# Kernel tuning notes

Measured on AMD Instinct MI355X. Metric: run time of the kernel, lower is better.

Reference implementation:

```python
import jax, jax.numpy as jnp
import numpy as np

RHO = 1e-8
EPS = 1e-8
THRESH = 0.9
MARK = -2


def maxi(x):
    # keep only the max entry along last dim, zero elsewhere
    idx = jnp.argmax(x, axis=-1, keepdims=True)
    return jnp.where(jnp.arange(x.shape[-1]) == idx, x, 0.0)


def argmaxi(x, eps=EPS):
    mx = jnp.abs(maxi(x))
    factors = jnp.max(mx, axis=-1, keepdims=True) - eps
    return mx / factors


def outer_forward(mm0, xs, rho=RHO):
    # mm0: (fields, mems, dim), xs: (batch, fields, dim)
    m = mm0 - 0.5
    x = xs - 0.5
    num = jnp.einsum('fmd,bfd->bfm', m, x) * 0.5
    m_norm = jnp.sqrt(jnp.sum(m * m, axis=-1))            # (f, m)
    x_norm = jnp.sqrt(jnp.sum(x * x, axis=-1))[..., None]  # (b, f, 1)
    return num / (m_norm[None] * x_norm + rho) + 0.5


def hidden_forward(mm, child_x, rho=RHO):
    # mm: (nodes, children, h_mems, c_mems), child_x: (batch, nodes*children, c_mems)
    n, c, hm, cm = mm.shape
    b = child_x.shape[0]
    x = maxi(child_x).reshape(b, n, c, cm)
    prop = jnp.einsum('nchk,bnck->bnh', mm, x)
    x_norm = jnp.sqrt(jnp.sum(x * x, axis=(2, 3)))[..., None]  # (b, n, 1)
    return prop / (c * x_norm + rho)


def mark_reserved_indices(acts, usages, trigger, mark=MARK):
    # acts: (b, n, m); usages: (n, m); trigger: (b, n, 1)
    res = jnp.argsort(acts, axis=-1)[:, :, -1:]        # argmax index, (b, n, 1)
    res = jnp.where(trigger, -1, res)
    res = res[:, :, 0].T                               # (n, b)
    sort_indices = jnp.argsort(usages, axis=-1)        # (n, m) ascending usage
    mask = res != -1                                   # (n, b)
    matches = ((res[:, :, None] == sort_indices[:, None, :]) & mask[:, :, None]).any(axis=1)  # (n, m)
    return jnp.where(matches, mark, sort_indices), sort_indices


def move_value_to_back(x, value=MARK):
    order = jnp.argsort((x == value).astype(jnp.int32), axis=-1)  # stable sort
    return jnp.take_along_axis(x, order, axis=-1)


def expand_for_batches(x, batch_size):
    n, m = x.shape
    full = batch_size // m + 1
    tiled = jnp.broadcast_to(x[None], (full, n, m)).transpose(1, 0, 2).reshape(n, -1)
    return tiled[:, :batch_size]


def growth_argmaxi(x, counts, eps=EPS, threshold=THRESH):
    b, n, m = x.shape
    normal = argmaxi(x, eps)
    trigger = jnp.sum(x > threshold, axis=-1, keepdims=True) <= 0  # (b, n, 1)
    avail, allidx = mark_reserved_indices(normal, counts, trigger, MARK)
    avail = move_value_to_back(avail, MARK)
    avail = expand_for_batches(avail, b)
    allidx = expand_for_batches(allidx, b)
    final = jnp.where(avail == MARK, allidx, avail)  # (n, b)
    idx = final.T.reshape(b, n, 1)
    vals = jnp.take_along_axis(x, idx, axis=-1)
    vals = jnp.where(vals == 0, 1.0, vals)
    gp = jnp.where(jnp.arange(m) == idx, vals, 0.0)  # scatter into zeros
    gp = argmaxi(jnp.abs(gp), eps)
    grown = jnp.where(trigger, gp, normal)
    uc = jnp.sum(grown, axis=0)
    uc = jnp.where(uc <= 0, counts, uc)
    return grown, uc


def setup_inputs() -> dict:
    key = jax.random.key(0)
    k1, k2, k3, k4 = jax.random.split(key, 4)
    xs = jax.random.uniform(k1, (32, 4096, 64), dtype=jnp.float32)
    mm0 = jax.random.uniform(k2, (4096, 64, 64), dtype=jnp.float32)
    mm1 = jax.random.normal(k3, (512, 8, 64, 64), dtype=jnp.float32) * 0.1
    mm2 = jax.random.normal(k4, (64, 8, 64, 64), dtype=jnp.float32) * 0.1
    counts = jnp.ones((64, 64), dtype=jnp.float32)
    return {'xs': xs, 'mm0': mm0, 'mm1': mm1, 'mm2': mm2, 'counts': counts}


def reference(xs, mm0, mm1, mm2, counts):
    h0 = outer_forward(mm0, xs)      # (b, 4096, 64)
    h1 = hidden_forward(mm1, h0)     # (b, 512, 64)
    h2 = hidden_forward(mm2, h1)     # (b, 64, 64)
    grown, _ = growth_argmaxi(h2, counts)
    return grown
```

## Files before the change

kernel.cpp:

```cpp
#include <hip/hip_runtime.h>
#include <cstdint>
#include <cstddef>

#define RHO 1e-8f
#define EPSV 1e-8f
#define THRESH 0.9f

typedef float v2f __attribute__((ext_vector_type(2)));

__device__ __forceinline__ float wave_max(float v) {
#pragma unroll
  for (int off = 1; off < 64; off <<= 1) v = fmaxf(v, __shfl_xor(v, off, 64));
  return v;
}

__global__ __launch_bounds__(128) void stage1_kernel(
    const float* __restrict__ xs, const float* __restrict__ mm0,
    float* __restrict__ maxv1, int* __restrict__ idx1) {
  const int lane = threadIdx.x & 63;
  const int wave = threadIdx.x >> 6;
  const int f = __builtin_amdgcn_readfirstlane(blockIdx.x * 2 + wave);

  __shared__ float mbuf[2][64 * 68];
  __shared__ float xbuf[2][32 * 68];
  float* mb = mbuf[wave];
  float* xb = xbuf[wave];

  const float* mf = mm0 + (size_t)f * 4096;
#pragma unroll
  for (int i = 0; i < 16; ++i) {
    const int g = i * 64 + lane;
    const int r = g >> 4, dq = g & 15;
    float4 v = *reinterpret_cast<const float4*>(mf + r * 64 + dq * 4);
    float4 w = {v.x - 0.5f, v.y - 0.5f, v.z - 0.5f, v.w - 0.5f};
    *reinterpret_cast<float4*>(&mb[r * 68 + dq * 4]) = w;
  }
  const float* xf = xs + (size_t)f * 64;
#pragma unroll
  for (int i = 0; i < 8; ++i) {
    const int g = i * 64 + lane;
    const int b = g >> 4, dq = g & 15;
    float4 v = *reinterpret_cast<const float4*>(xf + (size_t)b * (4096 * 64) + dq * 4);
    float4 w = {v.x - 0.5f, v.y - 0.5f, v.z - 0.5f, v.w - 0.5f};
    *reinterpret_cast<float4*>(&xb[b * 68 + dq * 4]) = w;
  }

  float mnv, xnv;
  {
    v2f s = {0.f, 0.f};
    const float* mr = &mb[lane * 68];
#pragma unroll
    for (int j = 0; j < 16; ++j) {
      float4 v = *reinterpret_cast<const float4*>(mr + 4 * j);
      s = (v2f){v.x, v.y} * (v2f){v.x, v.y} + s;
      s = (v2f){v.z, v.w} * (v2f){v.z, v.w} + s;
    }
    mnv = sqrtf(s.x + s.y);
  }
  {
    v2f s = {0.f, 0.f};
    const float* xr = &xb[(lane & 31) * 68];
#pragma unroll
    for (int j = 0; j < 16; ++j) {
      float4 v = *reinterpret_cast<const float4*>(xr + 4 * j);
      s = (v2f){v.x, v.y} * (v2f){v.x, v.y} + s;
      s = (v2f){v.z, v.w} * (v2f){v.z, v.w} + s;
    }
    xnv = sqrtf(s.x + s.y);
  }

  const int mg = lane >> 3, bg = lane & 7;
  v2f acc[8][4][2];
#pragma unroll
  for (int i = 0; i < 8; ++i)
#pragma unroll
    for (int j = 0; j < 4; ++j) {
      acc[i][j][0] = (v2f){0.f, 0.f};
      acc[i][j][1] = (v2f){0.f, 0.f};
    }

#pragma unroll
  for (int d0 = 0; d0 < 64; d0 += 4) {
    float4 a[8], bx[4];
#pragma unroll
    for (int i = 0; i < 8; ++i)
      a[i] = *reinterpret_cast<const float4*>(&mb[(mg + 8 * i) * 68 + d0]);
#pragma unroll
    for (int j = 0; j < 4; ++j)
      bx[j] = *reinterpret_cast<const float4*>(&xb[(bg + 8 * j) * 68 + d0]);
#pragma unroll
    for (int i = 0; i < 8; ++i)
#pragma unroll
      for (int j = 0; j < 4; ++j) {
        acc[i][j][0] = (v2f){a[i].x, a[i].y} * (v2f){bx[j].x, bx[j].y} + acc[i][j][0];
        acc[i][j][1] = (v2f){a[i].z, a[i].w} * (v2f){bx[j].z, bx[j].w} + acc[i][j][1];
      }
  }

  float mn_i[8], xn_j[4];
#pragma unroll
  for (int i = 0; i < 8; ++i) mn_i[i] = __shfl(mnv, mg + 8 * i, 64);
#pragma unroll
  for (int j = 0; j < 4; ++j) xn_j[j] = __shfl(xnv, bg + 8 * j, 64);

  float best[4];
  int bidx[4];
#pragma unroll
  for (int j = 0; j < 4; ++j) { best[j] = -__builtin_inff(); bidx[j] = 0; }
#pragma unroll
  for (int i = 0; i < 8; ++i)
#pragma unroll
    for (int j = 0; j < 4; ++j) {
      const float dot =
          acc[i][j][0].x + acc[i][j][0].y + acc[i][j][1].x + acc[i][j][1].y;
      const float val = (dot * 0.5f) / (mn_i[i] * xn_j[j] + RHO) + 0.5f;
      if (val > best[j]) { best[j] = val; bidx[j] = mg + 8 * i; }
    }
#pragma unroll
  for (int off = 8; off < 64; off <<= 1) {
#pragma unroll
    for (int j = 0; j < 4; ++j) {
      const float pv = __shfl_xor(best[j], off, 64);
      const int pm = __shfl_xor(bidx[j], off, 64);
      if (pv > best[j] || (pv == best[j] && pm < bidx[j])) {
        best[j] = pv; bidx[j] = pm;
      }
    }
  }
  if (mg == 0) {
#pragma unroll
    for (int j = 0; j < 4; ++j) {
      const int b = bg + 8 * j;
      maxv1[f * 32 + b] = best[j];
      idx1[f * 32 + b] = bidx[j];
    }
  }
}

#define STAGE_WRITE(T, R)                                    \
  do {                                                       \
    _Pragma("unroll") for (int i_ = 0; i_ < 4; ++i_) {       \
      const int g_ = tid + 256 * i_;                         \
      const int h_ = g_ >> 4, k0_ = (g_ & 15) * 4;           \
      (T)[(k0_ + 0) * 64 + (h_ ^ (k0_ + 0))] = (R)[i_].x;    \
      (T)[(k0_ + 1) * 64 + (h_ ^ (k0_ + 1))] = (R)[i_].y;    \
      (T)[(k0_ + 2) * 64 + (h_ ^ (k0_ + 2))] = (R)[i_].z;    \
      (T)[(k0_ + 3) * 64 + (h_ ^ (k0_ + 3))] = (R)[i_].w;    \
    }                                                        \
  } while (0)

#define LOAD_CHILD(R, C)                                     \
  do {                                                       \
    _Pragma("unroll") for (int i_ = 0; i_ < 4; ++i_)         \
        (R)[i_] = src[(C) * 1024 + tid + 256 * i_];          \
  } while (0)

#define COMPUTE_CHILD(C, T)                                              \
  do {                                                                   \
    _Pragma("unroll") for (int i_ = 0; i_ < 8; ++i_) {                   \
      const int b_ = wave * 8 + i_;                                      \
      const int off_ =                                                   \
          __builtin_amdgcn_readfirstlane((node * 8 + (C)) * 32 + b_);    \
      const int k_ = idx_in[off_];                                       \
      const float v_ = maxv_in[off_];                                    \
      const float w_ = (T)[k_ * 64 + (lane ^ k_)];                       \
      acc[i_] = fmaf(w_, v_, acc[i_]);                                   \
      s2[i_] = fmaf(v_, v_, s2[i_]);                                     \
    }                                                                    \
  } while (0)

__global__ __launch_bounds__(256) void stage2_kernel(
    const float* __restrict__ maxv_in, const int* __restrict__ idx_in,
    const float* __restrict__ mm,
    float* __restrict__ maxv_out, int* __restrict__ idx_out) {
  const int node = blockIdx.x;
  const int lane = threadIdx.x & 63;
  const int wave = threadIdx.x >> 6;
  const int tid = threadIdx.x;

  __shared__ float tA[4096], tB[4096];

  const float4* src = reinterpret_cast<const float4*>(mm + (size_t)node * (8 * 4096));

  float acc[8], s2[8];
#pragma unroll
  for (int i = 0; i < 8; ++i) { acc[i] = 0.f; s2[i] = 0.f; }

  float4 rE[4], rO[4];
  LOAD_CHILD(rE, 0);
  LOAD_CHILD(rO, 1);
  STAGE_WRITE(tA, rE);
  __syncthreads();

#pragma unroll
  for (int cc = 0; cc < 8; cc += 2) {
    if (cc + 2 < 8) LOAD_CHILD(rE, cc + 2);
    COMPUTE_CHILD(cc, tA);
    STAGE_WRITE(tB, rO);
    __syncthreads();
    if (cc + 3 < 8) LOAD_CHILD(rO, cc + 3);
    COMPUTE_CHILD(cc + 1, tB);
    if (cc + 2 < 8) {
      STAGE_WRITE(tA, rE);
    }
    __syncthreads();
  }

#pragma unroll
  for (int i = 0; i < 8; ++i) {
    const int b = wave * 8 + i;
    const float val = acc[i] / (8.f * sqrtf(s2[i]) + RHO);
    const float mx = wave_max(val);
    unsigned long long t = __ballot(val == mx);
    int j0 = __ffsll((long long)t) - 1;
    if (lane == 0) {
      maxv_out[node * 32 + b] = mx;
      idx_out[node * 32 + b] = j0;
    }
  }
}

__global__ __launch_bounds__(256) void grow_kernel(
    const float* __restrict__ maxv_in, const int* __restrict__ idx_in,
    const float* __restrict__ mm,
    const float* __restrict__ counts, float* __restrict__ out) {
  const int node = blockIdx.x;
  const int lane = threadIdx.x & 63;
  const int wave = threadIdx.x >> 6;
  const int tid = threadIdx.x;

  __shared__ float tA[4096], tB[4096];
  __shared__ float hbuf[32 * 64];
  __shared__ float mxvS[32];
  __shared__ int idxS[32];
  __shared__ int trgS[32];
  __shared__ float cntS[64];
  __shared__ int sidxS[64];
  __shared__ int flagS[64];
  __shared__ int compS[64];
  __shared__ int selS[32];
  __shared__ float valS[32];
  __shared__ int keptS[1];

  const float4* src = reinterpret_cast<const float4*>(mm + (size_t)node * (8 * 4096));

  float acc[8], s2[8];
#pragma unroll
  for (int i = 0; i < 8; ++i) { acc[i] = 0.f; s2[i] = 0.f; }

  float4 rE[4], rO[4];
  LOAD_CHILD(rE, 0);
  LOAD_CHILD(rO, 1);
  STAGE_WRITE(tA, rE);
  __syncthreads();

#pragma unroll
  for (int cc = 0; cc < 8; cc += 2) {
    if (cc + 2 < 8) LOAD_CHILD(rE, cc + 2);
    COMPUTE_CHILD(cc, tA);
    STAGE_WRITE(tB, rO);
    __syncthreads();
    if (cc + 3 < 8) LOAD_CHILD(rO, cc + 3);
    COMPUTE_CHILD(cc + 1, tB);
    if (cc + 2 < 8) {
      STAGE_WRITE(tA, rE);
    }
    __syncthreads();
  }

#pragma unroll
  for (int i = 0; i < 8; ++i) {
    const int b = wave * 8 + i;
    const float val = acc[i] / (8.f * sqrtf(s2[i]) + RHO);
    const float mx = wave_max(val);
    unsigned long long t = __ballot(val == mx);
    int j0 = __ffsll((long long)t) - 1;
    hbuf[b * 64 + lane] = val;
    unsigned long long big = __ballot(val > THRESH);
    if (lane == 0) {
      mxvS[b] = mx; idxS[b] = j0; trgS[b] = (big == 0ULL) ? 1 : 0;
    }
  }

  if (tid < 64) { cntS[tid] = counts[node * 64 + tid]; flagS[tid] = 0; }
  __syncthreads();
  if (tid < 64) {
    float cl = cntS[tid];
    int rank = 0;
    for (int j = 0; j < 64; ++j) {
      float cj = cntS[j];
      rank += (cj < cl || (cj == cl && j < tid)) ? 1 : 0;
    }
    sidxS[rank] = tid;
  }
  __syncthreads();
  if (tid < 32) {
    const int b = tid;
    if (!trgS[b]) {
      int j = idxS[b];
      float a = fabsf(mxvS[b]);
      int res;
      if (a > EPSV) res = j;
      else if (a == 0.f) res = 63;
      else if (a == EPSV) res = j;
      else res = (j == 63) ? 62 : 63;
      flagS[res] = 1;
    }
  }
  __syncthreads();
  if (wave == 0) {
    int s = sidxS[lane];
    int keep = flagS[s] ? 0 : 1;
    unsigned long long kb = __ballot(keep);
    int pos = __popcll(kb & ((1ULL << lane) - 1ULL));
    if (keep) compS[pos] = s;
    if (lane == 0) keptS[0] = __popcll(kb);
  }
  __syncthreads();
  if (tid < 32) {
    const int b = tid;
    int fin = (b < keptS[0]) ? compS[b] : sidxS[b];
    int idxb; float a;
    if (trgS[b]) {
      idxb = fin;
      float v = hbuf[b * 64 + idxb];
      if (v == 0.f) v = 1.f;
      a = fabsf(v);
    } else {
      idxb = idxS[b];
      a = fabsf(mxvS[b]);
    }
    selS[b] = idxb;
    valS[b] = a / (a - EPSV);
  }
  __syncthreads();
#pragma unroll
  for (int r = 0; r < 8; ++r) {
    int i = tid + 256 * r;
    int b = i >> 6, h = i & 63;
    out[((size_t)b * 64 + node) * 64 + h] = (h == selS[b]) ? valS[b] : 0.f;
  }
}

extern "C" void kernel_launch(void* const* d_in, const int* in_sizes, int n_in,
                              void* d_out, int out_size, void* d_ws, size_t ws_size,
                              hipStream_t stream) {
  const float* xs = (const float*)d_in[0];
  const float* mm0 = (const float*)d_in[1];
  const float* mm1 = (const float*)d_in[2];
  const float* mm2 = (const float*)d_in[3];
  const float* counts = (const float*)d_in[4];
  float* out = (float*)d_out;
  char* ws = (char*)d_ws;

  float* maxv1 = (float*)(ws + 0);
  int* idx1 = (int*)(ws + 524288);
  float* maxv2 = (float*)(ws + 1048576);
  int* idx2 = (int*)(ws + 1114112);

  stage1_kernel<<<dim3(2048), dim3(128), 0, stream>>>(xs, mm0, maxv1, idx1);
  stage2_kernel<<<dim3(512), dim3(256), 0, stream>>>(maxv1, idx1, mm1, maxv2, idx2);
  grow_kernel<<<dim3(64), dim3(256), 0, stream>>>(maxv2, idx2, mm2, counts, out);
}
```

Before: 215.0 us.

## Split stage1 field across two waves with swizzled LDS and stage child indices in LDS

Stage1 now assigns one field per 128-thread block, with the two waves splitting the 64 memory rows, instead of one field per wave. Padded LDS rows are replaced by an XOR-swizzled layout, and the norms are computed cooperatively and kept in shared memory. The per-wave argmax results are merged through LDS, which adds a barrier. Stage2 and grow now preload the child max values and indices into LDS in one coalesced load instead of doing scalar global loads inside the compute loop. The intent is to double the number of waves in flight and cut register pressure and global load latency, at the cost of extra syncs and a tie-break merge that must keep the lowest index on ties.

```diff
diff --git a/kernel.cpp b/kernel.cpp
--- a/kernel.cpp
+++ b/kernel.cpp
@@ -17,62 +17,58 @@
 __global__ __launch_bounds__(128) void stage1_kernel(
     const float* __restrict__ xs, const float* __restrict__ mm0,
     float* __restrict__ maxv1, int* __restrict__ idx1) {
-  const int lane = threadIdx.x & 63;
-  const int wave = threadIdx.x >> 6;
-  const int f = __builtin_amdgcn_readfirstlane(blockIdx.x * 2 + wave);
-
-  __shared__ float mbuf[2][64 * 68];
-  __shared__ float xbuf[2][32 * 68];
-  float* mb = mbuf[wave];
-  float* xb = xbuf[wave];
+  const int tid = threadIdx.x;
+  const int lane = tid & 63;
+  const int wave = tid >> 6;
+  const int f = blockIdx.x;
+
+  __shared__ float mS[64 * 64];
+  __shared__ float xS[32 * 64];
+  __shared__ float mnS[64];
+  __shared__ float xnS[32];
+  __shared__ float bestS[2][32];
+  __shared__ int bidxS[2][32];
 
   const float* mf = mm0 + (size_t)f * 4096;
 #pragma unroll
-  for (int i = 0; i < 16; ++i) {
-    const int g = i * 64 + lane;
-    const int r = g >> 4, dq = g & 15;
-    float4 v = *reinterpret_cast<const float4*>(mf + r * 64 + dq * 4);
+  for (int i = 0; i < 8; ++i) {
+    const int g = tid + 128 * i;
+    const int r = g >> 4, q = g & 15;
+    float4 v = *reinterpret_cast<const float4*>(mf + g * 4);
     float4 w = {v.x - 0.5f, v.y - 0.5f, v.z - 0.5f, v.w - 0.5f};
-    *reinterpret_cast<float4*>(&mb[r * 68 + dq * 4]) = w;
+    *reinterpret_cast<float4*>(&mS[(r * 16 + (q ^ (r & 15))) * 4]) = w;
   }
   const float* xf = xs + (size_t)f * 64;
 #pragma unroll
-  for (int i = 0; i < 8; ++i) {
-    const int g = i * 64 + lane;
-    const int b = g >> 4, dq = g & 15;
-    float4 v = *reinterpret_cast<const float4*>(xf + (size_t)b * (4096 * 64) + dq * 4);
+  for (int i = 0; i < 4; ++i) {
+    const int g = tid + 128 * i;
+    const int b = g >> 4, q = g & 15;
+    float4 v = *reinterpret_cast<const float4*>(xf + (size_t)b * (4096 * 64) + q * 4);
     float4 w = {v.x - 0.5f, v.y - 0.5f, v.z - 0.5f, v.w - 0.5f};
-    *reinterpret_cast<float4*>(&xb[b * 68 + dq * 4]) = w;
-  }
-
-  float mnv, xnv;
-  {
+    *reinterpret_cast<float4*>(&xS[(b * 16 + (q ^ (b & 15))) * 4]) = w;
+  }
+  __syncthreads();
+
+  if (tid < 96) {
+    const int r = (tid < 64) ? tid : (tid - 64);
+    const float* base = (tid < 64) ? mS : xS;
     v2f s = {0.f, 0.f};
-    const float* mr = &mb[lane * 68];
-#pragma unroll
-    for (int j = 0; j < 16; ++j) {
-      float4 v = *reinterpret_cast<const float4*>(mr + 4 * j);
+#pragma unroll
+    for (int q = 0; q < 16; ++q) {
+      float4 v = *reinterpret_cast<const float4*>(&base[(r * 16 + (q ^ (r & 15))) * 4]);
       s = (v2f){v.x, v.y} * (v2f){v.x, v.y} + s;
       s = (v2f){v.z, v.w} * (v2f){v.z, v.w} + s;
     }
-    mnv = sqrtf(s.x + s.y);
-  }
-  {
-    v2f s = {0.f, 0.f};
-    const float* xr = &xb[(lane & 31) * 68];
-#pragma unroll
-    for (int j = 0; j < 16; ++j) {
-      float4 v = *reinterpret_cast<const float4*>(xr + 4 * j);
-      s = (v2f){v.x, v.y} * (v2f){v.x, v.y} + s;
-      s = (v2f){v.z, v.w} * (v2f){v.z, v.w} + s;
-    }
-    xnv = sqrtf(s.x + s.y);
-  }
+    const float n = sqrtf(s.x + s.y);
+    if (tid < 64) mnS[r] = n; else xnS[r] = n;
+  }
+  __syncthreads();
 
   const int mg = lane >> 3, bg = lane & 7;
-  v2f acc[8][4][2];
-#pragma unroll
-  for (int i = 0; i < 8; ++i)
+  const int mrow0 = wave * 32 + mg;
+  v2f acc[4][4][2];
+#pragma unroll
+  for (int i = 0; i < 4; ++i)
 #pragma unroll
     for (int j = 0; j < 4; ++j) {
       acc[i][j][0] = (v2f){0.f, 0.f};
@@ -81,15 +77,20 @@
 
 #pragma unroll
   for (int d0 = 0; d0 < 64; d0 += 4) {
-    float4 a[8], bx[4];
-#pragma unroll
-    for (int i = 0; i < 8; ++i)
-      a[i] = *reinterpret_cast<const float4*>(&mb[(mg + 8 * i) * 68 + d0]);
-#pragma unroll
-    for (int j = 0; j < 4; ++j)
-      bx[j] = *reinterpret_cast<const float4*>(&xb[(bg + 8 * j) * 68 + d0]);
-#pragma unroll
-    for (int i = 0; i < 8; ++i)
+    const int q = d0 >> 2;
+    float4 a[4], bx[4];
+#pragma unroll
+    for (int i = 0; i < 4; ++i) {
+      const int r = mrow0 + 8 * i;
+      a[i] = *reinterpret_cast<const float4*>(&mS[(r * 16 + (q ^ (r & 15))) * 4]);
+    }
+#pragma unroll
+    for (int j = 0; j < 4; ++j) {
+      const int b = bg + 8 * j;
+      bx[j] = *reinterpret_cast<const float4*>(&xS[(b * 16 + (q ^ (b & 15))) * 4]);
+    }
+#pragma unroll
+    for (int i = 0; i < 4; ++i)
 #pragma unroll
       for (int j = 0; j < 4; ++j) {
         acc[i][j][0] = (v2f){a[i].x, a[i].y} * (v2f){bx[j].x, bx[j].y} + acc[i][j][0];
@@ -97,24 +98,24 @@
       }
   }
 
-  float mn_i[8], xn_j[4];
-#pragma unroll
-  for (int i = 0; i < 8; ++i) mn_i[i] = __shfl(mnv, mg + 8 * i, 64);
-#pragma unroll
-  for (int j = 0; j < 4; ++j) xn_j[j] = __shfl(xnv, bg + 8 * j, 64);
+  float mn_i[4], xn_j[4];
+#pragma unroll
+  for (int i = 0; i < 4; ++i) mn_i[i] = mnS[mrow0 + 8 * i];
+#pragma unroll
+  for (int j = 0; j < 4; ++j) xn_j[j] = xnS[bg + 8 * j];
 
   float best[4];
   int bidx[4];
 #pragma unroll
   for (int j = 0; j < 4; ++j) { best[j] = -__builtin_inff(); bidx[j] = 0; }
 #pragma unroll
-  for (int i = 0; i < 8; ++i)
+  for (int i = 0; i < 4; ++i)
 #pragma unroll
     for (int j = 0; j < 4; ++j) {
       const float dot =
           acc[i][j][0].x + acc[i][j][0].y + acc[i][j][1].x + acc[i][j][1].y;
       const float val = (dot * 0.5f) / (mn_i[i] * xn_j[j] + RHO) + 0.5f;
-      if (val > best[j]) { best[j] = val; bidx[j] = mg + 8 * i; }
+      if (val > best[j]) { best[j] = val; bidx[j] = mrow0 + 8 * i; }
     }
 #pragma unroll
   for (int off = 8; off < 64; off <<= 1) {
@@ -130,10 +131,17 @@
   if (mg == 0) {
 #pragma unroll
     for (int j = 0; j < 4; ++j) {
-      const int b = bg + 8 * j;
-      maxv1[f * 32 + b] = best[j];
-      idx1[f * 32 + b] = bidx[j];
-    }
+      bestS[wave][bg + 8 * j] = best[j];
+      bidxS[wave][bg + 8 * j] = bidx[j];
+    }
+  }
+  __syncthreads();
+  if (tid < 32) {
+    const float v0 = bestS[0][tid], v1 = bestS[1][tid];
+    const int i0 = bidxS[0][tid], i1 = bidxS[1][tid];
+    const bool take1 = (v1 > v0);
+    maxv1[f * 32 + tid] = take1 ? v1 : v0;
+    idx1[f * 32 + tid] = take1 ? i1 : i0;
   }
 }
 
@@ -159,10 +167,8 @@
   do {                                                                   \
     _Pragma("unroll") for (int i_ = 0; i_ < 8; ++i_) {                   \
       const int b_ = wave * 8 + i_;                                      \
-      const int off_ =                                                   \
-          __builtin_amdgcn_readfirstlane((node * 8 + (C)) * 32 + b_);    \
-      const int k_ = idx_in[off_];                                       \
-      const float v_ = maxv_in[off_];                                    \
+      const int k_ = ixL[(C) * 32 + b_];                                 \
+      const float v_ = mvL[(C) * 32 + b_];                               \
       const float w_ = (T)[k_ * 64 + (lane ^ k_)];                       \
       acc[i_] = fmaf(w_, v_, acc[i_]);                                   \
       s2[i_] = fmaf(v_, v_, s2[i_]);                                     \
@@ -179,8 +185,13 @@
   const int tid = threadIdx.x;
 
   __shared__ float tA[4096], tB[4096];
+  __shared__ float mvL[256];
+  __shared__ int ixL[256];
 
   const float4* src = reinterpret_cast<const float4*>(mm + (size_t)node * (8 * 4096));
+
+  mvL[tid] = maxv_in[node * 256 + tid];
+  ixL[tid] = idx_in[node * 256 + tid];
 
   float acc[8], s2[8];
 #pragma unroll
@@ -230,6 +241,8 @@
   const int tid = threadIdx.x;
 
   __shared__ float tA[4096], tB[4096];
+  __shared__ float mvL[256];
+  __shared__ int ixL[256];
   __shared__ float hbuf[32 * 64];
   __shared__ float mxvS[32];
   __shared__ int idxS[32];
@@ -243,6 +256,9 @@
   __shared__ int keptS[1];
 
   const float4* src = reinterpret_cast<const float4*>(mm + (size_t)node * (8 * 4096));
+
+  mvL[tid] = maxv_in[node * 256 + tid];
+  ixL[tid] = idx_in[node * 256 + tid];
 
   float acc[8], s2[8];
 #pragma unroll
@@ -358,7 +374,7 @@
   float* maxv2 = (float*)(ws + 1048576);
   int* idx2 = (int*)(ws + 1114112);
 
-  stage1_kernel<<<dim3(2048), dim3(128), 0, stream>>>(xs, mm0, maxv1, idx1);
+  stage1_kernel<<<dim3(4096), dim3(128), 0, stream>>>(xs, mm0, maxv1, idx1);
   stage2_kernel<<<dim3(512), dim3(256), 0, stream>>>(maxv1, idx1, mm1, maxv2, idx2);
   grow_kernel<<<dim3(64), dim3(256), 0, stream>>>(maxv2, idx2, mm2, counts, out);
 }
```

Measured after the change: 205.9 us. -4.2%, faster.
